# Kernel optimization log

Hardware: AMD Instinct MI355X
Metric: run time of the kernel (lower is better)

## Reference

```python
import jax, jax.numpy as jnp
import numpy as np

SIZE, SIGMA, N_RAD = 5, 0.6, 3  # kernel size, gaussian window sigma ('sfcnn'), radial shells 0..2

def radial_basis():
    # Gaussian radial window basis B_j(r) on the 5^3 grid, one shell per integer radius.
    c = (SIZE - 1) / 2.0
    ax = np.arange(SIZE, dtype=np.float64) - c
    X, Y, Z = np.meshgrid(ax, ax, ax, indexing='ij')
    r = np.sqrt(X**2 + Y**2 + Z**2)
    B = np.stack([np.exp(-0.5 * ((r - j) / SIGMA) ** 2) for j in range(N_RAD)])
    B = B / np.sqrt((B**2).sum(axis=(1, 2, 3), keepdims=True))  # sfcnn-style normalization
    return jnp.asarray(B, jnp.float32)  # [3,5,5,5]

def conv3d(x, k):
    # size-5 conv, stride 2, padding 3, NCDHW layout (as in the torch module)
    return jax.lax.conv_general_dilated(
        x, k, window_strides=(2, 2, 2), padding=[(3, 3)] * 3,
        dimension_numbers=('NCDHW', 'OIDHW', 'NCDHW'))

def highway_block(x, W, B, gated):
    # Kernel synthesized on-the-fly from radial basis: K[o,i] = sum_j W[o,i,j] * B_j
    k = jnp.einsum('oij,jxyz->oixyz', W, B)
    y = conv3d(x, k)
    if not gated:
        return y
    # capsule layout for features (5,1,1,1): 5 scalars | l1 (3) | l2 (5) | l3 (7) | 3 gate scalars
    scal = jax.nn.relu(y[:, :5])
    g = jax.nn.sigmoid(y[:, 20:23])
    l1 = y[:, 5:8] * g[:, 0:1]
    l2 = y[:, 8:13] * g[:, 1:2]
    l3 = y[:, 13:20] * g[:, 2:3]
    return jnp.concatenate([scal, l1, l2, l3], axis=1)

def setup_inputs() -> dict:
    key = jax.random.key(0)
    ks = jax.random.split(key, 8)
    inp = jax.random.normal(ks[0], (16, 1, 64, 64, 64), jnp.float32)
    # conv-kernel synthesis weights [out_ch, in_ch, n_radial]
    W0 = jax.random.normal(ks[1], (23, 1, N_RAD), jnp.float32) * (1.0 / np.sqrt(1 * N_RAD))
    W1 = jax.random.normal(ks[2], (23, 20, N_RAD), jnp.float32) * (1.0 / np.sqrt(20 * N_RAD))
    W2 = jax.random.normal(ks[3], (20, 20, N_RAD), jnp.float32) * (1.0 / np.sqrt(20 * N_RAD))
    fc1_w = jax.random.normal(ks[4], (50, 20), jnp.float32) * (1.0 / np.sqrt(20))
    fc1_b = jnp.zeros((50,), jnp.float32)
    fc2_w = jax.random.normal(ks[5], (2, 50), jnp.float32) * (1.0 / np.sqrt(50))
    fc2_b = jnp.zeros((2,), jnp.float32)
    return {'inp': inp, 'W0': W0, 'W1': W1, 'W2': W2,
            'fc1_w': fc1_w, 'fc1_b': fc1_b, 'fc2_w': fc2_w, 'fc2_b': fc2_b}

def reference(inp, W0, W1, W2, fc1_w, fc1_b, fc2_w, fc2_b):
    B = radial_basis()
    x = highway_block(inp, W0, B, gated=True)   # [B,20,33,33,33]
    x = highway_block(x, W1, B, gated=True)     # [B,20,18,18,18]
    x = highway_block(x, W2, B, gated=False)    # [B,20,10,10,10] (activation=None)
    x = x.reshape(x.shape[0], x.shape[1], -1).mean(-1)  # AvgSpacial -> [B,20]
    x = jax.nn.relu(x @ fc1_w.T + fc1_b)
    x = x @ fc2_w.T + fc2_b
    return x
```

## Files before the change

kernel.cpp:

```cpp
#include <hip/hip_runtime.h>
#include <math.h>
#include <type_traits>

constexpr int BATCH = 16;


__host__ __device__ constexpr int QI(int q) {
  return q == 0 ? 0 : q == 1 ? 1 : q == 2 ? 2 : q == 4 ? 3 : q == 5 ? 4 : 5;
}

template <int ICT, int DIN, int DOUT, int IRS, int MODE, int NBH>
__global__ __launch_bounds__(256)
void convA_kernel(const float* __restrict__ in, float* __restrict__ outp, int bofs) {
  constexpr int ISLAB = DIN * DIN * IRS;
  constexpr int XS = (DOUT + 1) / 2;
  constexpr int SPI = DOUT * DOUT * XS;
  constexpr int NB = (SPI + 255) / 256;
  constexpr int DOUT3 = DOUT * DOUT * DOUT;
  constexpr int XB = (NBH < 8) ? NBH : 8;
  static_assert(MODE == 0 || NB == 2, "S layout assumes 2 chunks");

  __shared__ __align__(16) float lbv[40];
  __shared__ float lnrm[4];
  __shared__ float red[4][3];

  const int bid = blockIdx.x;
  const int xcd = bid & 7;
  int slot = bid >> 3;
  const int chunk = slot % NB; slot /= NB;
  const int ic = slot % ICT;   slot /= ICT;
  const int brel = (xcd % XB) + XB * slot;
  const int b = brel + bofs;
  const int t = threadIdx.x;

  if (t < 40) {
    const int gc = t >> 2, j = t & 3;
    const float R2C[10] = {0.f, 1.f, 2.f, 3.f, 4.f, 5.f, 6.f, 8.f, 9.f, 12.f};
    float raw = 0.f;
    if (j < 3) {
      const float d = (sqrtf(R2C[gc]) - (float)j) * (1.0f / 0.6f);
      raw = expf(-0.5f * d * d);
    }
    lbv[t] = raw;
  }
  __syncthreads();
  if (t < 3) {
    const float MULT[10] = {1.f, 6.f, 12.f, 8.f, 6.f, 24.f, 24.f, 12.f, 24.f, 8.f};
    float ssum = 0.f;
    for (int gc = 0; gc < 10; ++gc) {
      const float v = lbv[gc * 4 + t];
      ssum += MULT[gc] * v * v;
    }
    lnrm[t] = rsqrtf(ssum);
  }
  __syncthreads();
  if (t < 40) lbv[t] = ((t & 3) < 3) ? lbv[t] * lnrm[t & 3] : 0.f;
  __syncthreads();

  const int s = chunk * 256 + t;
  const bool active = s < SPI;
  const int si = active ? s : 0;
  const int zo = si / (DOUT * XS);
  const int yo = (si / XS) % DOUT;
  const int xo0 = (si % XS) * 2;

  const float* __restrict__ ipc = in + (size_t)(b * ICT + ic) * ISLAB;
  const int offA = max(2 * xo0 - 4, 0);
  const int offB = min(2 * xo0, IRS - 4);
  bool xok[7];
#pragma unroll
  for (int p = 0; p < 7; ++p) xok[p] = (unsigned)(2 * xo0 - 3 + p) < (unsigned)DIN;
  int yoff[5];
  bool yok[5];
#pragma unroll
  for (int ky = 0; ky < 5; ++ky) {
    const int yi = 2 * yo - 3 + ky;
    yok[ky] = (unsigned)yi < (unsigned)DIN;
    yoff[ky] = min(max(yi, 0), DIN - 1) * IRS;
  }

  float z[3][2];
#pragma unroll
  for (int j = 0; j < 3; ++j) { z[j][0] = 0.f; z[j][1] = 0.f; }

  auto plane = [&](auto azc_c, int kz) {
    constexpr int AZC = decltype(azc_c)::value;
    constexpr int GM[3][6] = {
        {0, 1, 2, 4, 5, 7}, {1, 2, 3, 5, 6, 8}, {4, 5, 6, 7, 8, 9}};
    constexpr int A2T[5] = {4, 1, 0, 1, 4};
    const int zi = 2 * zo - 3 + kz;
    const bool zok = (unsigned)zi < (unsigned)DIN;
    const float* pl = ipc + (size_t)min(max(zi, 0), DIN - 1) * (DIN * IRS);
    float4 pa[5], pb[5];
#pragma unroll
    for (int ky = 0; ky < 5; ++ky) {
      const float* row = pl + yoff[ky];
      pa[ky] = *(const float4*)(row + offA);
      pb[ky] = *(const float4*)(row + offB);
    }
    float pq[6][2];
#pragma unroll
    for (int qi = 0; qi < 6; ++qi) { pq[qi][0] = 0.f; pq[qi][1] = 0.f; }
#pragma unroll
    for (int ky = 0; ky < 5; ++ky) {
      float v[7] = {pa[ky].y, pa[ky].z, pa[ky].w, pb[ky].x, pb[ky].y, pb[ky].z, pb[ky].w};
      const bool yz = zok && yok[ky];
#pragma unroll
      for (int p = 0; p < 7; ++p) v[p] = (yz && xok[p]) ? v[p] : 0.f;
#pragma unroll
      for (int kx = 0; kx < 5; ++kx) {
        pq[QI(A2T[ky] + A2T[kx])][0] += v[kx];
        pq[QI(A2T[ky] + A2T[kx])][1] += v[2 + kx];
      }
    }
#pragma unroll
    for (int qi = 0; qi < 6; ++qi) {
      const float4 bv4 = *(const float4*)&lbv[GM[AZC][qi] * 4];
#pragma unroll
      for (int n = 0; n < 2; ++n) {
        z[0][n] = fmaf(bv4.x, pq[qi][n], z[0][n]);
        z[1][n] = fmaf(bv4.y, pq[qi][n], z[1][n]);
        z[2][n] = fmaf(bv4.z, pq[qi][n], z[2][n]);
      }
    }
  };

  plane(std::integral_constant<int, 0>{}, 2);
#pragma unroll 1
  for (int rep = 0; rep < 2; ++rep) plane(std::integral_constant<int, 1>{}, 1 + 2 * rep);
#pragma unroll 1
  for (int rep = 0; rep < 2; ++rep) plane(std::integral_constant<int, 2>{}, 4 * rep);

  if constexpr (MODE == 0) {
    if (!active) return;
    const int vbase = (zo * DOUT + yo) * DOUT + xo0;
    float* __restrict__ zp = outp + ((size_t)(brel * ICT + ic) * 3) * DOUT3 + vbase;
#pragma unroll
    for (int j = 0; j < 3; ++j) {
      zp[(size_t)j * DOUT3] = z[j][0];
      if (xo0 + 1 < DOUT) zp[(size_t)j * DOUT3 + 1] = z[j][1];
    }
  } else {
    float v3[3];
#pragma unroll
    for (int j = 0; j < 3; ++j) v3[j] = active ? (z[j][0] + z[j][1]) : 0.f;
#pragma unroll
    for (int j = 0; j < 3; ++j) {
#pragma unroll
      for (int off = 32; off > 0; off >>= 1) v3[j] += __shfl_down(v3[j], off);
    }
    const int lane = t & 63, wv = t >> 6;
    if (lane == 0) {
#pragma unroll
      for (int j = 0; j < 3; ++j) red[wv][j] = v3[j];
    }
    __syncthreads();
    if (t < 3)
      outp[((size_t)(brel * ICT + ic) * 3 + t) * NB + chunk] =
          (red[0][t] + red[1][t]) + (red[2][t] + red[3][t]);
  }
}

template <int K, int DOUT, int ORS, int NBH>
__global__ __launch_bounds__(128)
void convB_kernel(const float* __restrict__ Z, const float* __restrict__ W,
                  float* __restrict__ out) {
  constexpr int ICT = K / 3;
  constexpr int DOUT3 = DOUT * DOUT * DOUT;
  constexpr int OSLAB = DOUT * DOUT * ORS;

  __shared__ __align__(16) float lw[K * 24];
  const int t = threadIdx.x;
  for (int i = t; i < K * 24; i += 128) {
    const int oc = i % 24, k = i / 24, icc = k / 3, jj = k % 3;
    lw[i] = (oc < 23) ? W[((size_t)oc * ICT + icc) * 3 + jj] : 0.f;
  }
  __syncthreads();

  const int gv = blockIdx.x * 128 + t;
  if (gv >= NBH * DOUT3) return;
  const int b = gv / DOUT3;
  const int vox = gv % DOUT3;

  float acc[24];
#pragma unroll
  for (int c = 0; c < 24; ++c) acc[c] = 0.f;

  const float* __restrict__ zp = Z + (size_t)b * K * DOUT3 + vox;
#pragma unroll 10
  for (int k = 0; k < K; ++k) {
    const float zv = zp[(size_t)k * DOUT3];
#pragma unroll
    for (int c4 = 0; c4 < 6; ++c4) {
      const float4 w4 = *(const float4*)&lw[k * 24 + 4 * c4];
      acc[c4 * 4 + 0] = fmaf(w4.x, zv, acc[c4 * 4 + 0]);
      acc[c4 * 4 + 1] = fmaf(w4.y, zv, acc[c4 * 4 + 1]);
      acc[c4 * 4 + 2] = fmaf(w4.z, zv, acc[c4 * 4 + 2]);
      acc[c4 * 4 + 3] = fmaf(w4.w, zv, acc[c4 * 4 + 3]);
    }
  }

  const int zz = vox / (DOUT * DOUT), yy = (vox / DOUT) % DOUT, xx = vox % DOUT;
  float* __restrict__ op = out + (size_t)b * 20 * OSLAB + (zz * DOUT + yy) * ORS + xx;
  const float g0 = 1.f / (1.f + expf(-acc[20]));
  const float g1 = 1.f / (1.f + expf(-acc[21]));
  const float g2 = 1.f / (1.f + expf(-acc[22]));
#pragma unroll
  for (int c = 0; c < 5; ++c) op[(size_t)c * OSLAB] = fmaxf(acc[c], 0.f);
#pragma unroll
  for (int c = 0; c < 3; ++c) op[(size_t)(5 + c) * OSLAB] = acc[5 + c] * g0;
#pragma unroll
  for (int c = 0; c < 5; ++c) op[(size_t)(8 + c) * OSLAB] = acc[8 + c] * g1;
#pragma unroll
  for (int c = 0; c < 7; ++c) op[(size_t)(13 + c) * OSLAB] = acc[13 + c] * g2;
}

__global__ __launch_bounds__(256)
void fc_kernel(const float* __restrict__ S, const float* __restrict__ W2,
               const float* __restrict__ fc1w, const float* __restrict__ fc1b,
               const float* __restrict__ fc2w, const float* __restrict__ fc2b,
               float* __restrict__ out) {
  const int t = threadIdx.x;
  __shared__ float SB[960];
  __shared__ float xs[320];
  __shared__ float hh[800];
  for (int i = t; i < 960; i += 256)
    SB[i] = S[(size_t)i * 2] + S[(size_t)i * 2 + 1];
  __syncthreads();
  for (int i = t; i < 320; i += 256) {
    const int b = i / 20, oc = i % 20;
    float s = 0.f;
    for (int k = 0; k < 60; ++k) s += W2[oc * 60 + k] * SB[b * 60 + k];
    xs[i] = s * (1.0f / 1000.0f);
  }
  __syncthreads();
  for (int i = t; i < 800; i += 256) {
    const int b = i / 50, j = i % 50;
    float s = fc1b[j];
    for (int c = 0; c < 20; ++c) s += xs[b * 20 + c] * fc1w[j * 20 + c];
    hh[i] = fmaxf(s, 0.f);
  }
  __syncthreads();
  for (int i = t; i < 32; i += 256) {
    const int b = i / 2, k = i % 2;
    float s = fc2b[k];
    for (int j = 0; j < 50; ++j) s += hh[b * 50 + j] * fc2w[k * 50 + j];
    out[b * 2 + k] = s;
  }
}

extern "C" void kernel_launch(void* const* d_in, const int* in_sizes, int n_in,
                              void* d_out, int out_size, void* d_ws, size_t ws_size,
                              hipStream_t stream) {
  (void)in_sizes; (void)n_in; (void)out_size;
  const float* inp  = (const float*)d_in[0];
  const float* W0   = (const float*)d_in[1];
  const float* W1   = (const float*)d_in[2];
  const float* W2   = (const float*)d_in[3];
  const float* fc1w = (const float*)d_in[4];
  const float* fc1b = (const float*)d_in[5];
  const float* fc2w = (const float*)d_in[6];
  const float* fc2b = (const float*)d_in[7];
  float* out = (float*)d_out;

  float* ws = (float*)d_ws;
  float* A0 = ws;
  float* A1 = A0 + (size_t)12545280;
  float* Z0 = A1;
  float* S  = A1 + (size_t)2073600;
  float* Z1 = S + 2048;

  const size_t favail = ws_size / 4;
  const size_t base = (size_t)12545280 + 2073600 + 2048;

  hipLaunchKernelGGL((convA_kernel<1, 64, 33, 64, 0, 16>), dim3(1168), dim3(256), 0, stream,
                     inp, Z0, 0);
  hipLaunchKernelGGL((convB_kernel<3, 33, 36, 16>), dim3(4493), dim3(128), 0, stream,
                     Z0, W0, A0);

  if (favail >= base + (size_t)16 * 60 * 5832) {
    hipLaunchKernelGGL((convA_kernel<20, 33, 18, 36, 0, 16>), dim3(3840), dim3(256), 0, stream,
                       A0, Z1, 0);
    hipLaunchKernelGGL((convB_kernel<60, 18, 20, 16>), dim3(729), dim3(128), 0, stream,
                       Z1, W1, A1);
  } else if (favail >= base + (size_t)8 * 60 * 5832) {
    for (int h = 0; h < 2; ++h) {
      hipLaunchKernelGGL((convA_kernel<20, 33, 18, 36, 0, 8>), dim3(1920), dim3(256), 0, stream,
                         A0, Z1, 8 * h);
      hipLaunchKernelGGL((convB_kernel<60, 18, 20, 8>), dim3(365), dim3(128), 0, stream,
                         Z1, W1, A1 + (size_t)8 * h * 20 * 6480);
    }
  } else {
    for (int h = 0; h < 4; ++h) {
      hipLaunchKernelGGL((convA_kernel<20, 33, 18, 36, 0, 4>), dim3(1920), dim3(256), 0, stream,
                         A0, Z1, 4 * h);
      hipLaunchKernelGGL((convB_kernel<60, 18, 20, 4>), dim3(183), dim3(128), 0, stream,
                         Z1, W1, A1 + (size_t)4 * h * 20 * 6480);
    }
  }

  hipLaunchKernelGGL((convA_kernel<20, 18, 10, 20, 1, 16>), dim3(640), dim3(256), 0, stream,
                     A1, S, 0);
  hipLaunchKernelGGL(fc_kernel, dim3(1), dim3(256), 0, stream, S, W2, fc1w, fc1b, fc2w, fc2b,
                     out);
}
```

Baseline: 88.57 us.

## Fuse first-layer radial conv and channel mixing with gating into one kernel

Replaces the two-kernel first layer (radial projection writing Z0, then convB mixing channels and applying gates) with a single conv0_kernel that computes the three radial responses per voxel and immediately applies W0, ReLU and sigmoid gating, writing A0 directly. This removes the intermediate Z0 round trip through global memory and one kernel launch. In exchange each thread holds a 24-wide accumulator and issues 20 strided stores, which raises register pressure and may reduce store coalescing. The shared basis and radial code is factored into helpers.

```diff
diff --git a/kernel.cpp b/kernel.cpp
--- a/kernel.cpp
+++ b/kernel.cpp
@@ -7,6 +7,173 @@
 
 __host__ __device__ constexpr int QI(int q) {
   return q == 0 ? 0 : q == 1 ? 1 : q == 2 ? 2 : q == 4 ? 3 : q == 5 ? 4 : 5;
+}
+
+__device__ __forceinline__ void synth_basis(float* lbv, float* lnrm, int t) {
+  if (t < 40) {
+    const int gc = t >> 2, j = t & 3;
+    const float R2C[10] = {0.f, 1.f, 2.f, 3.f, 4.f, 5.f, 6.f, 8.f, 9.f, 12.f};
+    float raw = 0.f;
+    if (j < 3) {
+      const float d = (sqrtf(R2C[gc]) - (float)j) * (1.0f / 0.6f);
+      raw = expf(-0.5f * d * d);
+    }
+    lbv[t] = raw;
+  }
+  __syncthreads();
+  if (t < 3) {
+    const float MULT[10] = {1.f, 6.f, 12.f, 8.f, 6.f, 24.f, 24.f, 12.f, 24.f, 8.f};
+    float ssum = 0.f;
+    for (int gc = 0; gc < 10; ++gc) {
+      const float v = lbv[gc * 4 + t];
+      ssum += MULT[gc] * v * v;
+    }
+    lnrm[t] = rsqrtf(ssum);
+  }
+  __syncthreads();
+  if (t < 40) lbv[t] = ((t & 3) < 3) ? lbv[t] * lnrm[t & 3] : 0.f;
+  __syncthreads();
+}
+
+template <int DIN, int DOUT, int IRS>
+__device__ __forceinline__ void radial_z(const float* __restrict__ ipc,
+                                         const float* __restrict__ lbv,
+                                         int zo, int yo, int xo0,
+                                         const bool* xok, const int* yoff,
+                                         const bool* yok, int offA, int offB,
+                                         float (&z)[3][2]) {
+#pragma unroll
+  for (int j = 0; j < 3; ++j) { z[j][0] = 0.f; z[j][1] = 0.f; }
+
+  auto plane = [&](auto azc_c, int kz) {
+    constexpr int AZC = decltype(azc_c)::value;
+    constexpr int GM[3][6] = {
+        {0, 1, 2, 4, 5, 7}, {1, 2, 3, 5, 6, 8}, {4, 5, 6, 7, 8, 9}};
+    constexpr int A2T[5] = {4, 1, 0, 1, 4};
+    const int zi = 2 * zo - 3 + kz;
+    const bool zok = (unsigned)zi < (unsigned)DIN;
+    const float* pl = ipc + (size_t)min(max(zi, 0), DIN - 1) * (DIN * IRS);
+    float4 pa[5], pb[5];
+#pragma unroll
+    for (int ky = 0; ky < 5; ++ky) {
+      const float* row = pl + yoff[ky];
+      pa[ky] = *(const float4*)(row + offA);
+      pb[ky] = *(const float4*)(row + offB);
+    }
+    float pq[6][2];
+#pragma unroll
+    for (int qi = 0; qi < 6; ++qi) { pq[qi][0] = 0.f; pq[qi][1] = 0.f; }
+#pragma unroll
+    for (int ky = 0; ky < 5; ++ky) {
+      float v[7] = {pa[ky].y, pa[ky].z, pa[ky].w, pb[ky].x, pb[ky].y, pb[ky].z, pb[ky].w};
+      const bool yz = zok && yok[ky];
+#pragma unroll
+      for (int p = 0; p < 7; ++p) v[p] = (yz && xok[p]) ? v[p] : 0.f;
+#pragma unroll
+      for (int kx = 0; kx < 5; ++kx) {
+        pq[QI(A2T[ky] + A2T[kx])][0] += v[kx];
+        pq[QI(A2T[ky] + A2T[kx])][1] += v[2 + kx];
+      }
+    }
+#pragma unroll
+    for (int qi = 0; qi < 6; ++qi) {
+      const float4 bv4 = *(const float4*)&lbv[GM[AZC][qi] * 4];
+#pragma unroll
+      for (int n = 0; n < 2; ++n) {
+        z[0][n] = fmaf(bv4.x, pq[qi][n], z[0][n]);
+        z[1][n] = fmaf(bv4.y, pq[qi][n], z[1][n]);
+        z[2][n] = fmaf(bv4.z, pq[qi][n], z[2][n]);
+      }
+    }
+  };
+
+  plane(std::integral_constant<int, 0>{}, 2);
+#pragma unroll 1
+  for (int rep = 0; rep < 2; ++rep) plane(std::integral_constant<int, 1>{}, 1 + 2 * rep);
+#pragma unroll 1
+  for (int rep = 0; rep < 2; ++rep) plane(std::integral_constant<int, 2>{}, 4 * rep);
+}
+
+__global__ __launch_bounds__(256)
+void conv0_kernel(const float* __restrict__ in, const float* __restrict__ W0,
+                  float* __restrict__ out) {
+  constexpr int DIN = 64, DOUT = 33, IRS = 64, ORS = 36;
+  constexpr int ISLAB = DIN * DIN * IRS;
+  constexpr int OSLAB = DOUT * DOUT * ORS;
+  constexpr int XS = 17, SPI = DOUT * DOUT * XS, NB = (SPI + 255) / 256;
+
+  __shared__ __align__(16) float lbv[40];
+  __shared__ float lnrm[4];
+  __shared__ __align__(16) float lw[3 * 24];
+
+  const int bid = blockIdx.x;
+  const int xcd = bid & 7;
+  int slot = bid >> 3;
+  const int chunk = slot % NB; slot /= NB;
+  const int b = xcd + 8 * slot;
+  const int t = threadIdx.x;
+
+  synth_basis(lbv, lnrm, t);
+  if (t < 72) {
+    const int oc = t % 24, j = t / 24;
+    lw[t] = (oc < 23) ? W0[oc * 3 + j] : 0.f;
+  }
+  __syncthreads();
+
+  const int s = chunk * 256 + t;
+  const bool active = s < SPI;
+  const int si = active ? s : 0;
+  const int zo = si / (DOUT * XS);
+  const int yo = (si / XS) % DOUT;
+  const int xo0 = (si % XS) * 2;
+
+  const float* __restrict__ ipc = in + (size_t)b * ISLAB;
+  const int offA = max(2 * xo0 - 4, 0);
+  const int offB = min(2 * xo0, IRS - 4);
+  bool xok[7];
+#pragma unroll
+  for (int p = 0; p < 7; ++p) xok[p] = (unsigned)(2 * xo0 - 3 + p) < (unsigned)DIN;
+  int yoff[5];
+  bool yok[5];
+#pragma unroll
+  for (int ky = 0; ky < 5; ++ky) {
+    const int yi = 2 * yo - 3 + ky;
+    yok[ky] = (unsigned)yi < (unsigned)DIN;
+    yoff[ky] = min(max(yi, 0), DIN - 1) * IRS;
+  }
+
+  float z[3][2];
+  radial_z<DIN, DOUT, IRS>(ipc, lbv, zo, yo, xo0, xok, yoff, yok, offA, offB, z);
+
+  if (!active) return;
+  float* __restrict__ op = out + (size_t)b * 20 * OSLAB + (zo * DOUT + yo) * ORS + xo0;
+#pragma unroll
+  for (int n = 0; n < 2; ++n) {
+    if (xo0 + n < DOUT) {
+      float acc[24];
+#pragma unroll
+      for (int c4 = 0; c4 < 6; ++c4) {
+        const float4 w0 = *(const float4*)&lw[0 * 24 + 4 * c4];
+        const float4 w1 = *(const float4*)&lw[1 * 24 + 4 * c4];
+        const float4 w2 = *(const float4*)&lw[2 * 24 + 4 * c4];
+        acc[c4 * 4 + 0] = w0.x * z[0][n] + w1.x * z[1][n] + w2.x * z[2][n];
+        acc[c4 * 4 + 1] = w0.y * z[0][n] + w1.y * z[1][n] + w2.y * z[2][n];
+        acc[c4 * 4 + 2] = w0.z * z[0][n] + w1.z * z[1][n] + w2.z * z[2][n];
+        acc[c4 * 4 + 3] = w0.w * z[0][n] + w1.w * z[1][n] + w2.w * z[2][n];
+      }
+      const float g0 = 1.f / (1.f + expf(-acc[20]));
+      const float g1 = 1.f / (1.f + expf(-acc[21]));
+      const float g2 = 1.f / (1.f + expf(-acc[22]));
+#pragma unroll
+      for (int c = 0; c < 5; ++c) op[(size_t)c * OSLAB + n] = fmaxf(acc[c], 0.f);
+#pragma unroll
+      for (int c = 0; c < 3; ++c) op[(size_t)(5 + c) * OSLAB + n] = acc[5 + c] * g0;
+#pragma unroll
+      for (int c = 0; c < 5; ++c) op[(size_t)(8 + c) * OSLAB + n] = acc[8 + c] * g1;
+#pragma unroll
+      for (int c = 0; c < 7; ++c) op[(size_t)(13 + c) * OSLAB + n] = acc[13 + c] * g2;
+    }
+  }
 }
 
 template <int ICT, int DIN, int DOUT, int IRS, int MODE, int NBH>
@@ -33,29 +200,7 @@
   const int b = brel + bofs;
   const int t = threadIdx.x;
 
-  if (t < 40) {
-    const int gc = t >> 2, j = t & 3;
-    const float R2C[10] = {0.f, 1.f, 2.f, 3.f, 4.f, 5.f, 6.f, 8.f, 9.f, 12.f};
-    float raw = 0.f;
-    if (j < 3) {
-      const float d = (sqrtf(R2C[gc]) - (float)j) * (1.0f / 0.6f);
-      raw = expf(-0.5f * d * d);
-    }
-    lbv[t] = raw;
-  }
-  __syncthreads();
-  if (t < 3) {
-    const float MULT[10] = {1.f, 6.f, 12.f, 8.f, 6.f, 24.f, 24.f, 12.f, 24.f, 8.f};
-    float ssum = 0.f;
-    for (int gc = 0; gc < 10; ++gc) {
-      const float v = lbv[gc * 4 + t];
-      ssum += MULT[gc] * v * v;
-    }
-    lnrm[t] = rsqrtf(ssum);
-  }
-  __syncthreads();
-  if (t < 40) lbv[t] = ((t & 3) < 3) ? lbv[t] * lnrm[t & 3] : 0.f;
-  __syncthreads();
+  synth_basis(lbv, lnrm, t);
 
   const int s = chunk * 256 + t;
   const bool active = s < SPI;
@@ -80,56 +225,7 @@
   }
 
   float z[3][2];
-#pragma unroll
-  for (int j = 0; j < 3; ++j) { z[j][0] = 0.f; z[j][1] = 0.f; }
-
-  auto plane = [&](auto azc_c, int kz) {
-    constexpr int AZC = decltype(azc_c)::value;
-    constexpr int GM[3][6] = {
-        {0, 1, 2, 4, 5, 7}, {1, 2, 3, 5, 6, 8}, {4, 5, 6, 7, 8, 9}};
-    constexpr int A2T[5] = {4, 1, 0, 1, 4};
-    const int zi = 2 * zo - 3 + kz;
-    const bool zok = (unsigned)zi < (unsigned)DIN;
-    const float* pl = ipc + (size_t)min(max(zi, 0), DIN - 1) * (DIN * IRS);
-    float4 pa[5], pb[5];
-#pragma unroll
-    for (int ky = 0; ky < 5; ++ky) {
-      const float* row = pl + yoff[ky];
-      pa[ky] = *(const float4*)(row + offA);
-      pb[ky] = *(const float4*)(row + offB);
-    }
-    float pq[6][2];
-#pragma unroll
-    for (int qi = 0; qi < 6; ++qi) { pq[qi][0] = 0.f; pq[qi][1] = 0.f; }
-#pragma unroll
-    for (int ky = 0; ky < 5; ++ky) {
-      float v[7] = {pa[ky].y, pa[ky].z, pa[ky].w, pb[ky].x, pb[ky].y, pb[ky].z, pb[ky].w};
-      const bool yz = zok && yok[ky];
-#pragma unroll
-      for (int p = 0; p < 7; ++p) v[p] = (yz && xok[p]) ? v[p] : 0.f;
-#pragma unroll
-      for (int kx = 0; kx < 5; ++kx) {
-        pq[QI(A2T[ky] + A2T[kx])][0] += v[kx];
-        pq[QI(A2T[ky] + A2T[kx])][1] += v[2 + kx];
-      }
-    }
-#pragma unroll
-    for (int qi = 0; qi < 6; ++qi) {
-      const float4 bv4 = *(const float4*)&lbv[GM[AZC][qi] * 4];
-#pragma unroll
-      for (int n = 0; n < 2; ++n) {
-        z[0][n] = fmaf(bv4.x, pq[qi][n], z[0][n]);
-        z[1][n] = fmaf(bv4.y, pq[qi][n], z[1][n]);
-        z[2][n] = fmaf(bv4.z, pq[qi][n], z[2][n]);
-      }
-    }
-  };
-
-  plane(std::integral_constant<int, 0>{}, 2);
-#pragma unroll 1
-  for (int rep = 0; rep < 2; ++rep) plane(std::integral_constant<int, 1>{}, 1 + 2 * rep);
-#pragma unroll 1
-  for (int rep = 0; rep < 2; ++rep) plane(std::integral_constant<int, 2>{}, 4 * rep);
+  radial_z<DIN, DOUT, IRS>(ipc, lbv, zo, yo, xo0, xok, yoff, yok, offA, offB, z);
 
   if constexpr (MODE == 0) {
     if (!active) return;
@@ -266,17 +362,13 @@
   float* ws = (float*)d_ws;
   float* A0 = ws;
   float* A1 = A0 + (size_t)12545280;
-  float* Z0 = A1;
   float* S  = A1 + (size_t)2073600;
   float* Z1 = S + 2048;
 
   const size_t favail = ws_size / 4;
   const size_t base = (size_t)12545280 + 2073600 + 2048;
 
-  hipLaunchKernelGGL((convA_kernel<1, 64, 33, 64, 0, 16>), dim3(1168), dim3(256), 0, stream,
-                     inp, Z0, 0);
-  hipLaunchKernelGGL((convB_kernel<3, 33, 36, 16>), dim3(4493), dim3(128), 0, stream,
-                     Z0, W0, A0);
+  hipLaunchKernelGGL(conv0_kernel, dim3(1168), dim3(256), 0, stream, inp, W0, A0);
 
   if (favail >= base + (size_t)16 * 60 * 5832) {
     hipLaunchKernelGGL((convA_kernel<20, 33, 18, 36, 0, 16>), dim3(3840), dim3(256), 0, stream,
```

Result: faster. 82.84 us, median of 2 (-6.5%).
